# Performance work log

Measured on AMD Instinct MI355X. Metric: run time of the kernel, lower is better.

## Reference

```python
import jax, jax.numpy as jnp
import numpy as np

B, L, D = 8, 2048, 64   # batch, length, input_dim
K, NU = 40, 32          # num scales, reservoir units
LEAKY = 0.0
REG = 1.0


def setup_inputs() -> dict:
    key = jax.random.key(0)
    k1, k2 = jax.random.split(key)
    x = jax.random.normal(k1, (B, L, D), dtype=jnp.float32)
    radii = jax.random.uniform(k2, (K,), dtype=jnp.float32, minval=0.1, maxval=0.99)
    rng = np.random.default_rng(0)
    W_in = jnp.asarray(rng.standard_normal((D, NU)).astype(np.float32))
    # uni_res=True: one sparse reservoir, spectral-radius normalized, repeated K times
    connectivity = min(1.0, 10.0 / NU)
    w = rng.standard_normal((NU, NU)) * (rng.random((NU, NU)) < connectivity)
    w = w / np.max(np.abs(np.linalg.eigvals(w)))
    W_res = jnp.asarray(np.repeat(w[None].astype(np.float32), K, axis=0))
    return {"x": x, "radii": radii, "W_in": W_in, "W_res": W_res}


def reference(x, radii, W_in, W_res):
    Bb, Ll, Dd = x.shape
    k, nu = W_res.shape[0], W_res.shape[1]
    T = Ll - 1
    xt = x @ W_in                                # [B,L,nu]
    Wr = W_res * radii[:, None, None]            # [k,nu,nu]
    ar = jnp.arange(k)

    # Multi-scale recurrence: scale r reads its own state delayed by r+1 steps.
    # Rolling buffer buf[:, r, j] holds column (t-1-j) of scale r's history, so
    # h_pre for scale r is the diagonal buf[:, r, r] (== h_history[:, r, t-r-1];
    # zero for t-r-1 < 0, matching the torch code's untouched zero init).
    def step(buf, x_t):                          # buf [B,k,k,nu], x_t [B,nu]
        h_pre = buf[:, ar, ar, :]                # [B,k,nu] diagonal gather
        h_t = x_t[:, None, :] + jnp.einsum('brn,rnm->brm', h_pre, Wr)
        new = LEAKY * h_pre + (1.0 - LEAKY) * jnp.tanh(h_t)
        buf = jnp.concatenate([new[:, :, None, :], buf[:, :, :-1, :]], axis=2)
        return buf, new

    buf0 = jnp.zeros((Bb, k, k, nu), x.dtype)
    _, hist = jax.lax.scan(step, buf0, jnp.swapaxes(xt[:, :T], 0, 1))
    h_hist = jnp.transpose(hist, (1, 2, 0, 3))   # [B,k,T,nu]

    # Scale i has L-1-i valid timesteps; mask instead of ragged slicing.
    t_idx = jnp.arange(T)
    mask = (t_idx[None, :] < (Ll - 1 - ar)[:, None]).astype(x.dtype)  # [k,T]
    Hm = h_hist * mask[None, :, :, None]          # [B,k,T,nu]
    idx = jnp.minimum(t_idx[None, :] + ar[:, None] + 1, Ll - 1)       # [k,T]
    Xm = x[:, idx, :] * mask[None, :, :, None]    # [B,k,T,D] (x shifted by i+1)

    eye = REG * jnp.eye(nu, dtype=x.dtype)
    HtH = jnp.einsum('bktn,bktm->bknm', Hm, Hm) + eye   # [B,k,nu,nu]
    HtX = jnp.einsum('bktn,bktd->bknd', Hm, Xm)         # [B,k,nu,D]
    W_out = jnp.linalg.solve(HtH, HtX)                  # [B,k,nu,D]

    err = jnp.einsum('bktn,bknd->bktd', Hm, W_out) - Xm
    f_norms = jnp.sum(err, axis=(0, 2, 3))              # [k]
    features = W_out.reshape(Bb, k, nu * Dd)            # [B,k,nu*D]
    return features, f_norms
```

## Files before the change

### kernel.cpp

```cpp
#include <hip/hip_runtime.h>

#define B_ 8
#define L_ 2048
#define D_ 64
#define K_ 40
#define NU_ 32
#define T_ 2047
#define NSPLIT 8

#define XT_OFF   0
#define XT_SZ    (B_*L_*NU_)
#define HH_OFF   (XT_OFF + XT_SZ)
#define HH_SZ    (B_*K_*T_*NU_)
#define HTHP_OFF (HH_OFF + HH_SZ)
#define HTHP_SZ  (NSPLIT*B_*K_*NU_*NU_)
#define HTXP_OFF (HTHP_OFF + HTHP_SZ)
#define HTXP_SZ  (NSPLIT*B_*K_*NU_*D_)
#define SH_OFF   (HTXP_OFF + HTXP_SZ)
#define SH_SZ    (B_*K_*NU_)
#define SX_OFF   (SH_OFF + SH_SZ)
#define SX_SZ    (B_*K_)

#if __has_builtin(__builtin_amdgcn_exp2f)
#define EXP2F(x) __builtin_amdgcn_exp2f(x)
#else
#define EXP2F(x) __expf((x)*0.6931471805599453f)
#endif
#if __has_builtin(__builtin_amdgcn_rcpf)
#define RCPF(x) __builtin_amdgcn_rcpf(x)
#else
#define RCPF(x) (1.0f/(x))
#endif

__global__ __launch_bounds__(256) void k1_xt(const float* __restrict__ x,
                                             const float* __restrict__ Win,
                                             float* __restrict__ xt)
{
    __shared__ float Ws[D_*NU_];
    for (int i = threadIdx.x; i < D_*NU_; i += 256) Ws[i] = Win[i];
    __syncthreads();
    int gid = blockIdx.x*256 + threadIdx.x;
    int m   = gid & 31;
    int row = gid >> 5;
    const float4* xr = (const float4*)(x + (size_t)row * 64);
    float s = 0.f;
#pragma unroll
    for (int q = 0; q < 16; ++q) {
        float4 v = xr[q];
        s = fmaf(v.x, Ws[(q*4+0)*32+m], s);
        s = fmaf(v.y, Ws[(q*4+1)*32+m], s);
        s = fmaf(v.z, Ws[(q*4+2)*32+m], s);
        s = fmaf(v.w, Ws[(q*4+3)*32+m], s);
    }
    xt[gid] = s;
}

#define BPV(N) __int_as_float(__builtin_amdgcn_ds_bpermute(pbase + ((N)<<2), hb))

#define STEP(XV, SD) { \
    float a0 = XV, a1 = 0.f, a2 = 0.f, a3 = 0.f; \
    a0 = fmaf(w0,  BPV(0),  a0); a1 = fmaf(w1,  BPV(1),  a1); \
    a2 = fmaf(w2,  BPV(2),  a2); a3 = fmaf(w3,  BPV(3),  a3); \
    a0 = fmaf(w4,  BPV(4),  a0); a1 = fmaf(w5,  BPV(5),  a1); \
    a2 = fmaf(w6,  BPV(6),  a2); a3 = fmaf(w7,  BPV(7),  a3); \
    a0 = fmaf(w8,  BPV(8),  a0); a1 = fmaf(w9,  BPV(9),  a1); \
    a2 = fmaf(w10, BPV(10), a2); a3 = fmaf(w11, BPV(11), a3); \
    a0 = fmaf(w12, BPV(12), a0); a1 = fmaf(w13, BPV(13), a1); \
    a2 = fmaf(w14, BPV(14), a2); a3 = fmaf(w15, BPV(15), a3); \
    a0 = fmaf(w16, BPV(16), a0); a1 = fmaf(w17, BPV(17), a1); \
    a2 = fmaf(w18, BPV(18), a2); a3 = fmaf(w19, BPV(19), a3); \
    a0 = fmaf(w20, BPV(20), a0); a1 = fmaf(w21, BPV(21), a1); \
    a2 = fmaf(w22, BPV(22), a2); a3 = fmaf(w23, BPV(23), a3); \
    a0 = fmaf(w24, BPV(24), a0); a1 = fmaf(w25, BPV(25), a1); \
    a2 = fmaf(w26, BPV(26), a2); a3 = fmaf(w27, BPV(27), a3); \
    a0 = fmaf(w28, BPV(28), a0); a1 = fmaf(w29, BPV(29), a1); \
    a2 = fmaf(w30, BPV(30), a2); a3 = fmaf(w31, BPV(31), a3); \
    float sdot = (a0 + a1) + (a2 + a3); \
    float ex = EXP2F(sdot * 2.8853900817779268f); \
    SD = fmaf(-2.f, RCPF(ex + 1.f), 1.f); \
    hb = __float_as_int(SD); }

#define CHUNK(XC, XN, ST) { \
    XN##0 = xnp[0];               XN##1 = xnp[(size_t)1*adv]; \
    XN##2 = xnp[(size_t)2*adv];   XN##3 = xnp[(size_t)3*adv]; \
    XN##4 = xnp[(size_t)4*adv];   XN##5 = xnp[(size_t)5*adv]; \
    XN##6 = xnp[(size_t)6*adv];   XN##7 = xnp[(size_t)7*adv]; \
    xnp += 8*(size_t)adv; \
    STEP(XC##0, ST##0) STEP(XC##1, ST##1) STEP(XC##2, ST##2) STEP(XC##3, ST##3) \
    STEP(XC##4, ST##4) STEP(XC##5, ST##5) STEP(XC##6, ST##6) STEP(XC##7, ST##7) \
    if (srem >= 8) { \
        hq[0]             = ST##0; hq[(size_t)1*adv] = ST##1; \
        hq[(size_t)2*adv] = ST##2; hq[(size_t)3*adv] = ST##3; \
        hq[(size_t)4*adv] = ST##4; hq[(size_t)5*adv] = ST##5; \
        hq[(size_t)6*adv] = ST##6; hq[(size_t)7*adv] = ST##7; \
    } else { \
        if (srem > 0) hq[0]             = ST##0; \
        if (srem > 1) hq[(size_t)1*adv] = ST##1; \
        if (srem > 2) hq[(size_t)2*adv] = ST##2; \
        if (srem > 3) hq[(size_t)3*adv] = ST##3; \
        if (srem > 4) hq[(size_t)4*adv] = ST##4; \
        if (srem > 5) hq[(size_t)5*adv] = ST##5; \
        if (srem > 6) hq[(size_t)6*adv] = ST##6; \
    } \
    hq += 8*(size_t)adv; srem -= 8; }

__global__ __launch_bounds__(64, 2) void k2_rec(const float* __restrict__ ws_xt,
                                                const float* __restrict__ Wres,
                                                const float* __restrict__ radii,
                                                float* __restrict__ hh)
{
    const int l    = threadIdx.x;
    const int m    = l & 31;
    const int half = l >> 5;
    const int pbase = half << 7;
    int e = blockIdx.x % 820;
    int q = blockIdx.x / 820;
    const int b = 2*q + half;
    int r = 0, base = 0;
    while (e >= base + r + 1) { base += r + 1; ++r; }
    const int cc     = e - base;
    const int stride = r + 1;
    const float rad  = radii[r];

    if (r == 0)      __builtin_amdgcn_s_setprio(3);
    else if (r <= 2) __builtin_amdgcn_s_setprio(2);
    else if (r <= 6) __builtin_amdgcn_s_setprio(1);

    const float* Wp = Wres + r*1024 + m;
    float w0  = Wp[0*32]*rad,  w1  = Wp[1*32]*rad,  w2  = Wp[2*32]*rad,  w3  = Wp[3*32]*rad;
    float w4  = Wp[4*32]*rad,  w5  = Wp[5*32]*rad,  w6  = Wp[6*32]*rad,  w7  = Wp[7*32]*rad;
    float w8  = Wp[8*32]*rad,  w9  = Wp[9*32]*rad,  w10 = Wp[10*32]*rad, w11 = Wp[11*32]*rad;
    float w12 = Wp[12*32]*rad, w13 = Wp[13*32]*rad, w14 = Wp[14*32]*rad, w15 = Wp[15*32]*rad;
    float w16 = Wp[16*32]*rad, w17 = Wp[17*32]*rad, w18 = Wp[18*32]*rad, w19 = Wp[19*32]*rad;
    float w20 = Wp[20*32]*rad, w21 = Wp[21*32]*rad, w22 = Wp[22*32]*rad, w23 = Wp[23*32]*rad;
    float w24 = Wp[24*32]*rad, w25 = Wp[25*32]*rad, w26 = Wp[26*32]*rad, w27 = Wp[27*32]*rad;
    float w28 = Wp[28*32]*rad, w29 = Wp[29*32]*rad, w30 = Wp[30*32]*rad, w31 = Wp[31*32]*rad;

    const int nsteps = (T_ - 1 - cc) / stride + 1;
    const int adv = stride * NU_;
    const float* xnp = ws_xt + (size_t)b * L_ * NU_ + (size_t)cc * NU_ + m;
    float* hq = hh + ((size_t)(b*K_ + r) * T_ + cc) * NU_ + m;

    float xa0 = xnp[0],             xa1 = xnp[(size_t)1*adv],
          xa2 = xnp[(size_t)2*adv], xa3 = xnp[(size_t)3*adv],
          xa4 = xnp[(size_t)4*adv], xa5 = xnp[(size_t)5*adv],
          xa6 = xnp[(size_t)6*adv], xa7 = xnp[(size_t)7*adv];
    xnp += 8*(size_t)adv;
    float xb0=0,xb1=0,xb2=0,xb3=0,xb4=0,xb5=0,xb6=0,xb7=0;
    float sa0,sa1,sa2,sa3,sa4,sa5,sa6,sa7;
    float sb0,sb1,sb2,sb3,sb4,sb5,sb6,sb7;

    int hb = 0;
    int srem = nsteps;
    const int nchunks = (nsteps + 7) >> 3;
    int c = 0;
    for (; c + 2 <= nchunks; c += 2) {
        CHUNK(xa, xb, sa)
        CHUNK(xb, xa, sb)
    }
    if (c < nchunks) CHUNK(xa, xb, sa)
}

__global__ __launch_bounds__(64) void k3_gemm(const float* __restrict__ hh,
                                              const float* __restrict__ x,
                                              float* __restrict__ htHp,
                                              float* __restrict__ htXp,
                                              float* __restrict__ sH,
                                              float* __restrict__ sX)
{
    const int s  = blockIdx.x;
    const int k  = blockIdx.y;
    const int b  = blockIdx.z;
    const int l  = threadIdx.x;
    const int bk = b*K_ + k;
    const int Tk = T_ - k;
    __shared__ __align__(16) float P[32][96];
    const int tidn = l / 12;
    const int tidc = l % 12;

    float acc[8][8];
#pragma unroll
    for (int i = 0; i < 8; ++i)
#pragma unroll
        for (int j = 0; j < 8; ++j) acc[i][j] = 0.f;
    float bsum[8];
#pragma unroll
    for (int j = 0; j < 8; ++j) bsum[j] = 0.f;

    const float* hrow = hh + (size_t)bk * T_ * NU_;
    const float* xrow = x + (size_t)b * L_ * D_ + (size_t)(k+1) * D_;

    for (int ch = s*8; ch < s*8 + 8; ++ch) {
        const int t0 = ch*32;
#pragma unroll
        for (int rd = 0; rd < 12; ++rd) {
            int slot = rd*64 + l;
            int row  = slot / 24;
            int q    = slot % 24;
            int tt   = t0 + row;
            float4 v = make_float4(0.f, 0.f, 0.f, 0.f);
            if (tt < Tk) {
                if (q < 8) v = *(const float4*)(hrow + (size_t)tt*32 + q*4);
                else       v = *(const float4*)(xrow + (size_t)tt*64 + (q-8)*4);
            }
            *(float4*)&P[row][q*4] = v;
        }
        __syncthreads();
        if (l < 48) {
#pragma unroll 4
            for (int tt = 0; tt < 32; ++tt) {
                const float* pr = &P[tt][0];
                float4 A0 = *(const float4*)(pr + tidn*8);
                float4 A1 = *(const float4*)(pr + tidn*8 + 4);
                float4 B0 = *(const float4*)(pr + tidc*8);
                float4 B1 = *(const float4*)(pr + tidc*8 + 4);
                float av[8] = {A0.x,A0.y,A0.z,A0.w,A1.x,A1.y,A1.z,A1.w};
                float bv[8] = {B0.x,B0.y,B0.z,B0.w,B1.x,B1.y,B1.z,B1.w};
#pragma unroll
                for (int i = 0; i < 8; ++i)
#pragma unroll
                    for (int j = 0; j < 8; ++j)
                        acc[i][j] = fmaf(av[i], bv[j], acc[i][j]);
#pragma unroll
                for (int j = 0; j < 8; ++j) bsum[j] += bv[j];
            }
        }
        __syncthreads();
    }
    if (l < 48) {
        const int base_h = (s*(B_*K_) + bk)*NU_*NU_;
        const int base_x = (s*(B_*K_) + bk)*NU_*D_;
#pragma unroll
        for (int i = 0; i < 8; ++i) {
            int n = tidn*8 + i;
#pragma unroll
            for (int j = 0; j < 8; ++j) {
                int c = tidc*8 + j;
                if (c < 32) htHp[base_h + n*32 + c]      = acc[i][j];
                else        htXp[base_x + n*64 + (c-32)] = acc[i][j];
            }
        }
        if (tidn == 0) {
            if (tidc < 4) {
#pragma unroll
                for (int j = 0; j < 8; ++j)
                    atomicAdd(&sH[bk*32 + tidc*8 + j], bsum[j]);
            } else {
                float t = 0.f;
#pragma unroll
                for (int j = 0; j < 8; ++j) t += bsum[j];
                atomicAdd(&sX[bk], t);
            }
        }
    }
}

__global__ __launch_bounds__(64) void k4_solve(const float* __restrict__ htHp,
                                               const float* __restrict__ htXp,
                                               const float* __restrict__ sH,
                                               const float* __restrict__ sX,
                                               float* __restrict__ dout)
{
    const int k  = blockIdx.x;
    const int b  = blockIdx.y;
    const int bk = b*K_ + k;
    const int l  = threadIdx.x;
    __shared__ float As[32][33];
#pragma unroll
    for (int i = 0; i < 16; ++i) {
        int idx = i*64 + l;
        int row = idx >> 5, col = idx & 31;
        float v = (row == col) ? 1.0f : 0.0f;
        for (int s2 = 0; s2 < NSPLIT; ++s2)
            v += htHp[(size_t)(s2*(B_*K_) + bk)*1024 + idx];
        As[row][col] = v;
    }
    __syncthreads();
    for (int j = 0; j < 32; ++j) {
        float d   = sqrtf(As[j][j]);
        float inv = 1.0f / d;
        if (l == j) As[j][j] = d;
        if (l < 32 && l > j) As[l][j] *= inv;
        __syncthreads();
        if (l < 32 && l > j) {
            float lij = As[l][j];
            for (int c = j+1; c <= l; ++c)
                As[l][c] -= lij * As[c][j];
        }
        __syncthreads();
    }
    float y[32];
#pragma unroll
    for (int i = 0; i < 32; ++i) {
        float v = 0.f;
        for (int s2 = 0; s2 < NSPLIT; ++s2)
            v += htXp[(size_t)(s2*(B_*K_) + bk)*2048 + i*64 + l];
        y[i] = v;
    }
#pragma unroll
    for (int i = 0; i < 32; ++i) {
        float v = y[i];
#pragma unroll
        for (int j = 0; j < i; ++j) v = fmaf(-As[i][j], y[j], v);
        y[i] = v / As[i][i];
    }
#pragma unroll
    for (int i = 31; i >= 0; --i) {
        float v = y[i];
#pragma unroll
        for (int j = i+1; j < 32; ++j) v = fmaf(-As[j][i], y[j], v);
        y[i] = v / As[i][i];
    }
    float* fout = dout + (size_t)bk * NU_ * D_;
#pragma unroll
    for (int n = 0; n < 32; ++n) fout[n*64 + l] = y[n];
    const float* sh = sH + bk*32;
    float part = 0.f;
#pragma unroll
    for (int n = 0; n < 32; ++n) part = fmaf(sh[n], y[n], part);
#pragma unroll
    for (int off = 32; off > 0; off >>= 1) part += __shfl_xor(part, off);
    if (l == 0) atomicAdd(dout + (size_t)(B_*K_*NU_*D_) + k, part - sX[bk]);
}

extern "C" void kernel_launch(void* const* d_in, const int* in_sizes, int n_in,
                              void* d_out, int out_size, void* d_ws, size_t ws_size,
                              hipStream_t stream)
{
    const float* x     = (const float*)d_in[0];
    const float* radii = (const float*)d_in[1];
    const float* Win   = (const float*)d_in[2];
    const float* Wres  = (const float*)d_in[3];
    float* ws   = (float*)d_ws;
    float* xt   = ws + XT_OFF;
    float* hh   = ws + HH_OFF;
    float* htHp = ws + HTHP_OFF;
    float* htXp = ws + HTXP_OFF;
    float* sH   = ws + SH_OFF;
    float* sX   = ws + SX_OFF;
    float* out  = (float*)d_out;

    hipMemsetAsync(sH, 0, (size_t)(SH_SZ + SX_SZ)*sizeof(float), stream);
    hipMemsetAsync(out + (size_t)B_*K_*NU_*D_, 0, K_*sizeof(float), stream);

    k1_xt <<<(B_*L_*NU_)/256, 256, 0, stream>>>(x, Win, xt);
    k2_rec<<<4*820, 64, 0, stream>>>(xt, Wres, radii, hh);
    k3_gemm<<<dim3(NSPLIT, K_, B_), 64, 0, stream>>>(hh, x, htHp, htXp, sH, sX);
    k4_solve<<<dim3(K_, B_), 64, 0, stream>>>(htHp, htXp, sH, sX, out);
}
```

Before: 935.6 us.

## Fuse recurrence and Gram kernels with per-scale completion counters

The recurrence and Gram-accumulation kernels are merged into one launch. Gram blocks spin on per-(batch,scale) atomic counters until every recurrence block for that scale has finished, so Gram work on early-finishing scales overlaps the long-running recurrence chains. The time split for the Gram stage drops from 8 to 4. Spin-waiting blocks take CU slots and depend on the recurrence blocks being scheduled first, and the k4 reduction now sees fewer partial sums.

```diff
diff --git a/kernel.cpp b/kernel.cpp
--- a/kernel.cpp
+++ b/kernel.cpp
@@ -6,7 +6,9 @@
 #define K_ 40
 #define NU_ 32
 #define T_ 2047
-#define NSPLIT 8
+#define NSPLIT 4
+#define NK2B 3280
+#define NK3B (NSPLIT*K_*B_)
 
 #define XT_OFF   0
 #define XT_SZ    (B_*L_*NU_)
@@ -20,6 +22,8 @@
 #define SH_SZ    (B_*K_*NU_)
 #define SX_OFF   (SH_OFF + SH_SZ)
 #define SX_SZ    (B_*K_)
+#define CNT_OFF  (SX_OFF + SX_SZ)
+#define CNT_SZ   (B_*K_)
 
 #if __has_builtin(__builtin_amdgcn_exp2f)
 #define EXP2F(x) __builtin_amdgcn_exp2f(x)
@@ -104,76 +108,89 @@
     } \
     hq += 8*(size_t)adv; srem -= 8; }
 
-__global__ __launch_bounds__(64, 2) void k2_rec(const float* __restrict__ ws_xt,
-                                                const float* __restrict__ Wres,
-                                                const float* __restrict__ radii,
-                                                float* __restrict__ hh)
+__global__ __launch_bounds__(64, 2) void k23(const float* __restrict__ ws_xt,
+                                             const float* __restrict__ Wres,
+                                             const float* __restrict__ radii,
+                                             float* __restrict__ hh,
+                                             const float* __restrict__ x,
+                                             float* __restrict__ htHp,
+                                             float* __restrict__ htXp,
+                                             float* __restrict__ sH,
+                                             float* __restrict__ sX,
+                                             int*   __restrict__ cnt)
 {
-    const int l    = threadIdx.x;
-    const int m    = l & 31;
-    const int half = l >> 5;
-    const int pbase = half << 7;
-    int e = blockIdx.x % 820;
-    int q = blockIdx.x / 820;
-    const int b = 2*q + half;
-    int r = 0, base = 0;
-    while (e >= base + r + 1) { base += r + 1; ++r; }
-    const int cc     = e - base;
-    const int stride = r + 1;
-    const float rad  = radii[r];
-
-    if (r == 0)      __builtin_amdgcn_s_setprio(3);
-    else if (r <= 2) __builtin_amdgcn_s_setprio(2);
-    else if (r <= 6) __builtin_amdgcn_s_setprio(1);
-
-    const float* Wp = Wres + r*1024 + m;
-    float w0  = Wp[0*32]*rad,  w1  = Wp[1*32]*rad,  w2  = Wp[2*32]*rad,  w3  = Wp[3*32]*rad;
-    float w4  = Wp[4*32]*rad,  w5  = Wp[5*32]*rad,  w6  = Wp[6*32]*rad,  w7  = Wp[7*32]*rad;
-    float w8  = Wp[8*32]*rad,  w9  = Wp[9*32]*rad,  w10 = Wp[10*32]*rad, w11 = Wp[11*32]*rad;
-    float w12 = Wp[12*32]*rad, w13 = Wp[13*32]*rad, w14 = Wp[14*32]*rad, w15 = Wp[15*32]*rad;
-    float w16 = Wp[16*32]*rad, w17 = Wp[17*32]*rad, w18 = Wp[18*32]*rad, w19 = Wp[19*32]*rad;
-    float w20 = Wp[20*32]*rad, w21 = Wp[21*32]*rad, w22 = Wp[22*32]*rad, w23 = Wp[23*32]*rad;
-    float w24 = Wp[24*32]*rad, w25 = Wp[25*32]*rad, w26 = Wp[26*32]*rad, w27 = Wp[27*32]*rad;
-    float w28 = Wp[28*32]*rad, w29 = Wp[29*32]*rad, w30 = Wp[30*32]*rad, w31 = Wp[31*32]*rad;
-
-    const int nsteps = (T_ - 1 - cc) / stride + 1;
-    const int adv = stride * NU_;
-    const float* xnp = ws_xt + (size_t)b * L_ * NU_ + (size_t)cc * NU_ + m;
-    float* hq = hh + ((size_t)(b*K_ + r) * T_ + cc) * NU_ + m;
-
-    float xa0 = xnp[0],             xa1 = xnp[(size_t)1*adv],
-          xa2 = xnp[(size_t)2*adv], xa3 = xnp[(size_t)3*adv],
-          xa4 = xnp[(size_t)4*adv], xa5 = xnp[(size_t)5*adv],
-          xa6 = xnp[(size_t)6*adv], xa7 = xnp[(size_t)7*adv];
-    xnp += 8*(size_t)adv;
-    float xb0=0,xb1=0,xb2=0,xb3=0,xb4=0,xb5=0,xb6=0,xb7=0;
-    float sa0,sa1,sa2,sa3,sa4,sa5,sa6,sa7;
-    float sb0,sb1,sb2,sb3,sb4,sb5,sb6,sb7;
-
-    int hb = 0;
-    int srem = nsteps;
-    const int nchunks = (nsteps + 7) >> 3;
-    int c = 0;
-    for (; c + 2 <= nchunks; c += 2) {
-        CHUNK(xa, xb, sa)
-        CHUNK(xb, xa, sb)
-    }
-    if (c < nchunks) CHUNK(xa, xb, sa)
-}
-
-__global__ __launch_bounds__(64) void k3_gemm(const float* __restrict__ hh,
-                                              const float* __restrict__ x,
-                                              float* __restrict__ htHp,
-                                              float* __restrict__ htXp,
-                                              float* __restrict__ sH,
-                                              float* __restrict__ sX)
-{
-    const int s  = blockIdx.x;
-    const int k  = blockIdx.y;
-    const int b  = blockIdx.z;
-    const int l  = threadIdx.x;
+    const int l = threadIdx.x;
+    if (blockIdx.x < NK2B) {
+        const int m    = l & 31;
+        const int half = l >> 5;
+        const int pbase = half << 7;
+        int e = blockIdx.x % 820;
+        int q = blockIdx.x / 820;
+        const int b = 2*q + half;
+        int r = 0, base = 0;
+        while (e >= base + r + 1) { base += r + 1; ++r; }
+        const int cc     = e - base;
+        const int stride = r + 1;
+        const float rad  = radii[r];
+
+        if (r == 0)      __builtin_amdgcn_s_setprio(3);
+        else if (r <= 2) __builtin_amdgcn_s_setprio(2);
+        else if (r <= 6) __builtin_amdgcn_s_setprio(1);
+
+        const float* Wp = Wres + r*1024 + m;
+        float w0  = Wp[0*32]*rad,  w1  = Wp[1*32]*rad,  w2  = Wp[2*32]*rad,  w3  = Wp[3*32]*rad;
+        float w4  = Wp[4*32]*rad,  w5  = Wp[5*32]*rad,  w6  = Wp[6*32]*rad,  w7  = Wp[7*32]*rad;
+        float w8  = Wp[8*32]*rad,  w9  = Wp[9*32]*rad,  w10 = Wp[10*32]*rad, w11 = Wp[11*32]*rad;
+        float w12 = Wp[12*32]*rad, w13 = Wp[13*32]*rad, w14 = Wp[14*32]*rad, w15 = Wp[15*32]*rad;
+        float w16 = Wp[16*32]*rad, w17 = Wp[17*32]*rad, w18 = Wp[18*32]*rad, w19 = Wp[19*32]*rad;
+        float w20 = Wp[20*32]*rad, w21 = Wp[21*32]*rad, w22 = Wp[22*32]*rad, w23 = Wp[23*32]*rad;
+        float w24 = Wp[24*32]*rad, w25 = Wp[25*32]*rad, w26 = Wp[26*32]*rad, w27 = Wp[27*32]*rad;
+        float w28 = Wp[28*32]*rad, w29 = Wp[29*32]*rad, w30 = Wp[30*32]*rad, w31 = Wp[31*32]*rad;
+
+        const int nsteps = (T_ - 1 - cc) / stride + 1;
+        const int adv = stride * NU_;
+        const float* xnp = ws_xt + (size_t)b * L_ * NU_ + (size_t)cc * NU_ + m;
+        float* hq = hh + ((size_t)(b*K_ + r) * T_ + cc) * NU_ + m;
+
+        float xa0 = xnp[0],             xa1 = xnp[(size_t)1*adv],
+              xa2 = xnp[(size_t)2*adv], xa3 = xnp[(size_t)3*adv],
+              xa4 = xnp[(size_t)4*adv], xa5 = xnp[(size_t)5*adv],
+              xa6 = xnp[(size_t)6*adv], xa7 = xnp[(size_t)7*adv];
+        xnp += 8*(size_t)adv;
+        float xb0=0,xb1=0,xb2=0,xb3=0,xb4=0,xb5=0,xb6=0,xb7=0;
+        float sa0,sa1,sa2,sa3,sa4,sa5,sa6,sa7;
+        float sb0,sb1,sb2,sb3,sb4,sb5,sb6,sb7;
+
+        int hb = 0;
+        int srem = nsteps;
+        const int nchunks = (nsteps + 7) >> 3;
+        int c = 0;
+        for (; c + 2 <= nchunks; c += 2) {
+            CHUNK(xa, xb, sa)
+            CHUNK(xb, xa, sb)
+        }
+        if (c < nchunks) CHUNK(xa, xb, sa)
+
+        __threadfence();
+        if ((l & 31) == 0)
+            __hip_atomic_fetch_add(&cnt[b*K_ + r], 1, __ATOMIC_RELAXED,
+                                   __HIP_MEMORY_SCOPE_AGENT);
+        return;
+    }
+
+    const int idx2 = blockIdx.x - NK2B;
+    const int s  = idx2 & (NSPLIT-1);
+    const int k  = K_-1 - ((idx2/NSPLIT) % K_);
+    const int b  = idx2 / (NSPLIT*K_);
     const int bk = b*K_ + k;
     const int Tk = T_ - k;
+    const int need = k + 1;
+
+    while (__hip_atomic_load(&cnt[bk], __ATOMIC_RELAXED,
+                             __HIP_MEMORY_SCOPE_AGENT) < need)
+        __builtin_amdgcn_s_sleep(16);
+    __threadfence();
+
     __shared__ __align__(16) float P[32][96];
     const int tidn = l / 12;
     const int tidc = l % 12;
@@ -190,7 +207,8 @@
     const float* hrow = hh + (size_t)bk * T_ * NU_;
     const float* xrow = x + (size_t)b * L_ * D_ + (size_t)(k+1) * D_;
 
-    for (int ch = s*8; ch < s*8 + 8; ++ch) {
+    const int CPS = 64 / NSPLIT;
+    for (int ch = s*CPS; ch < s*CPS + CPS; ++ch) {
         const int t0 = ch*32;
 #pragma unroll
         for (int rd = 0; rd < 12; ++rd) {
@@ -338,13 +356,14 @@
     float* htXp = ws + HTXP_OFF;
     float* sH   = ws + SH_OFF;
     float* sX   = ws + SX_OFF;
+    int*   cnt  = (int*)(ws + CNT_OFF);
     float* out  = (float*)d_out;
 
-    hipMemsetAsync(sH, 0, (size_t)(SH_SZ + SX_SZ)*sizeof(float), stream);
+    hipMemsetAsync(sH, 0, (size_t)(SH_SZ + SX_SZ + CNT_SZ)*sizeof(float), stream);
     hipMemsetAsync(out + (size_t)B_*K_*NU_*D_, 0, K_*sizeof(float), stream);
 
-    k1_xt <<<(B_*L_*NU_)/256, 256, 0, stream>>>(x, Win, xt);
-    k2_rec<<<4*820, 64, 0, stream>>>(xt, Wres, radii, hh);
-    k3_gemm<<<dim3(NSPLIT, K_, B_), 64, 0, stream>>>(hh, x, htHp, htXp, sH, sX);
+    k1_xt<<<(B_*L_*NU_)/256, 256, 0, stream>>>(x, Win, xt);
+    k23  <<<NK2B + NK3B, 64, 0, stream>>>(xt, Wres, radii, hh, x,
+                                          htHp, htXp, sH, sX, cnt);
     k4_solve<<<dim3(K_, B_), 64, 0, stream>>>(htHp, htXp, sH, sX, out);
 }
```

After: 1.035 ms. 10.7% more time.
